# Kernel optimization log

Hardware: AMD Instinct MI355X
Metric: run time of the kernel (lower is better)

Reference implementation:

```python
import jax, jax.numpy as jnp
import numpy as np

ALPHA = -10.0  # softmax sharpness on |x - bin| distances
TAU = 0.0
TAU2 = 0.0
EPS = 1e-10

B, F, L, K = 32, 64, 1024, 32


def setup_inputs() -> dict:
    key = jax.random.key(0)
    k1, k2 = jax.random.split(key)
    x = jax.random.normal(k1, (B, F, L), dtype=jnp.float32)
    bins = jax.random.normal(k2, (K,), dtype=jnp.float32)
    return {"x": x, "bins": bins}


def reference(x, bins):
    # dist: [B, F, L, K] = |x[..., None] - bins|
    dist = jnp.abs(x[..., None] - bins)
    # soft assignment over the K bins (training path of the module)
    soft = jax.nn.softmax(ALPHA * dist, axis=-1)
    assignment = soft + EPS

    # weighted quantization loss: sum of per-bin mean of sqrt(assignment)
    quant = jnp.sum(jnp.mean(jnp.sqrt(assignment), axis=(0, 1, 2)))
    weighted_quant_loss = jnp.stack([quant, jnp.float32(TAU2)])[None, :]  # [1, 2]

    # code entropy of average assignment distribution
    p = jnp.mean(assignment, axis=(0, 1, 2))  # [K]
    code_entropy = -jnp.sum(p * jnp.log(p))
    weighted_code_entropy = jnp.stack([code_entropy, jnp.float32(TAU)])[None, :]  # [1, 2]

    # soft reconstruction against the bins: [B, F, L]
    bit_code = jnp.einsum('bflk,k->bfl', assignment, bins)
    return bit_code, weighted_code_entropy, weighted_quant_loss
```

## Files before the change

kernel.cpp:

```cpp
#include <hip/hip_runtime.h>

#define K      32
#define TPB    256
#define NB     2048
#define EPT    4
#define NTOT   (32 * 64 * 1024)
#define STRIDE (TPB * NB)

typedef float v2f __attribute__((ext_vector_type(2)));

__device__ __forceinline__ float wave_reduce_sum(float v) {
#pragma unroll
  for (int m = 1; m < 64; m <<= 1) v += __shfl_xor(v, m, 64);
  return v;
}

__device__ __forceinline__ float to_sgpr(float v) {
  return __int_as_float(__builtin_amdgcn_readfirstlane(__float_as_int(v)));
}

__global__ __launch_bounds__(TPB)
void ssq_main(const float* __restrict__ x, const float* __restrict__ bins,
              float* __restrict__ out, float* __restrict__ partials) {
  const int tid  = threadIdx.x;
  const int base = blockIdx.x * TPB + tid;

  float binv[K];
#pragma unroll
  for (int k = 0; k < K; ++k) binv[k] = to_sgpr(bins[k]);
  float binsum = 0.f;
#pragma unroll
  for (int k = 0; k < K; ++k) binsum += binv[k];
  const float epsb = 1e-10f * binsum;

  v2f binv2[K / 2];
#pragma unroll
  for (int i = 0; i < K / 2; ++i) binv2[i] = (v2f){binv[2 * i], binv[2 * i + 1]};

  float xs[EPT];
#pragma unroll
  for (int e = 0; e < EPT; ++e) xs[e] = x[base + e * STRIDE];

  v2f sAcc2[K / 2];
#pragma unroll
  for (int i = 0; i < K / 2; ++i) sAcc2[i] = (v2f){0.f, 0.f};
  float q = 0.f;

  const float Ch = -7.213475204444817f;
  const v2f Ch2 = {Ch, Ch};

#pragma unroll 1
  for (int e = 0; e < EPT; ++e) {
    const float xv = xs[e];
    const v2f xv2 = {xv, xv};
    v2f t2[K / 2];
    v2f s2a = {0.f, 0.f}, s2b = {0.f, 0.f};
    v2f h2a = {0.f, 0.f}, h2b = {0.f, 0.f};
    v2f b2a = {0.f, 0.f}, b2b = {0.f, 0.f};
#pragma unroll
    for (int i = 0; i < K / 2; i += 2) {
      v2f d0 = xv2 - binv2[i];
      v2f d1 = xv2 - binv2[i + 1];
      v2f p0 = d0 * Ch2;
      v2f p1 = d1 * Ch2;
      v2f m0 = __builtin_elementwise_min(p0, -p0);
      v2f m1 = __builtin_elementwise_min(p1, -p1);
      v2f h0 = {__builtin_amdgcn_exp2f(m0.x), __builtin_amdgcn_exp2f(m0.y)};
      v2f h1 = {__builtin_amdgcn_exp2f(m1.x), __builtin_amdgcn_exp2f(m1.y)};
      v2f t0 = h0 * h0;
      v2f t1 = h1 * h1;
      t2[i]     = t0;
      t2[i + 1] = t1;
      s2a += t0; s2b += t1;
      h2a += h0; h2b += h1;
      b2a += t0 * binv2[i];
      b2b += t1 * binv2[i + 1];
    }
    const v2f sv2 = (s2a + s2b);
    const v2f hv2 = (h2a + h2b);
    const v2f bv2 = (b2a + b2b);
    const float s    = sv2.x + sv2.y;
    const float hsum = hv2.x + hv2.y;
    const float bnum = bv2.x + bv2.y;
    const float inv  = __builtin_amdgcn_rcpf(s);
    q = fmaf(hsum, __builtin_amdgcn_rsqf(s), q);
    out[base + e * STRIDE] = fmaf(bnum, inv, epsb);
    const v2f inv2 = {inv, inv};
#pragma unroll
    for (int i = 0; i < K / 2; ++i) sAcc2[i] += t2[i] * inv2;
  }

  __shared__ float red[4][K + 1];
  const int lane = tid & 63, wv = tid >> 6;
#pragma unroll
  for (int k = 0; k < K; ++k) {
    float v = wave_reduce_sum(sAcc2[k >> 1][k & 1]);
    if (lane == 0) red[wv][k] = v;
  }
  {
    float v = wave_reduce_sum(q);
    if (lane == 0) red[wv][K] = v;
  }
  __syncthreads();
  if (tid < K + 1) {
    float v = red[0][tid] + red[1][tid] + red[2][tid] + red[3][tid];
    partials[tid * NB + blockIdx.x] = v;
  }
}

__global__ __launch_bounds__(TPB)
void ssq_reduce(const float* __restrict__ partials, float* __restrict__ sums) {
  const float* p = partials + blockIdx.x * NB;
  const int tid  = threadIdx.x;
  float s = 0.f;
#pragma unroll
  for (int j = 0; j < NB / TPB; ++j) s += p[tid + j * TPB];
  s = wave_reduce_sum(s);
  __shared__ float red[4];
  if ((tid & 63) == 0) red[tid >> 6] = s;
  __syncthreads();
  if (tid == 0) sums[blockIdx.x] = red[0] + red[1] + red[2] + red[3];
}

__global__ void ssq_final(const float* __restrict__ sums, float* __restrict__ out) {
  const int lane = threadIdx.x;
  float e = 0.f;
  if (lane < K) {
    float p = sums[lane] * (1.0f / (float)NTOT) + 1e-10f;
    e = -p * __logf(p);
  }
  e = wave_reduce_sum(e);
  if (lane == 0) {
    out[NTOT + 0] = e;
    out[NTOT + 1] = 0.f;
    out[NTOT + 2] = sums[K] * (1.0f / (float)NTOT);
    out[NTOT + 3] = 0.f;
  }
}

extern "C" void kernel_launch(void* const* d_in, const int* in_sizes, int n_in,
                              void* d_out, int out_size, void* d_ws, size_t ws_size,
                              hipStream_t stream) {
  const float* x    = (const float*)d_in[0];
  const float* bins = (const float*)d_in[1];
  float* out        = (float*)d_out;
  float* partials   = (float*)d_ws;
  float* sums       = partials + (K + 1) * NB;

  ssq_main  <<<NB,    TPB, 0, stream>>>(x, bins, out, partials);
  ssq_reduce<<<K + 1, TPB, 0, stream>>>(partials, sums);
  ssq_final <<<1,     64,  0, stream>>>(sums, out);
}
```

Baseline: 88.07 us.

## Fuse reduction kernels into main kernel via last-block atomic counter

Merges the three-kernel pipeline into a single kernel. Each block bumps an atomic counter after writing its partials, and the last block to finish reduces all partials and computes the entropy and quantization outputs. Halves the grid to 1024 blocks with 8 elements per thread so there are fewer partials, and unrolls the element loop by 2. This removes two kernel launches at the cost of a memset, a serial tail reduction run by one block, and higher register pressure from the unroll.

```diff
diff --git a/kernel.cpp b/kernel.cpp
--- a/kernel.cpp
+++ b/kernel.cpp
@@ -2,8 +2,8 @@
 
 #define K      32
 #define TPB    256
-#define NB     2048
-#define EPT    4
+#define NB     1024
+#define EPT    8
 #define NTOT   (32 * 64 * 1024)
 #define STRIDE (TPB * NB)
 
@@ -20,8 +20,9 @@
 }
 
 __global__ __launch_bounds__(TPB)
-void ssq_main(const float* __restrict__ x, const float* __restrict__ bins,
-              float* __restrict__ out, float* __restrict__ partials) {
+void ssq_fused(const float* __restrict__ x, const float* __restrict__ bins,
+               float* __restrict__ out, float* __restrict__ partials,
+               unsigned int* __restrict__ counter) {
   const int tid  = threadIdx.x;
   const int base = blockIdx.x * TPB + tid;
 
@@ -49,7 +50,7 @@
   const float Ch = -7.213475204444817f;
   const v2f Ch2 = {Ch, Ch};
 
-#pragma unroll 1
+#pragma unroll 2
   for (int e = 0; e < EPT; ++e) {
     const float xv = xs[e];
     const v2f xv2 = {xv, xv};
@@ -106,34 +107,36 @@
     float v = red[0][tid] + red[1][tid] + red[2][tid] + red[3][tid];
     partials[tid * NB + blockIdx.x] = v;
   }
-}
 
-__global__ __launch_bounds__(TPB)
-void ssq_reduce(const float* __restrict__ partials, float* __restrict__ sums) {
-  const float* p = partials + blockIdx.x * NB;
-  const int tid  = threadIdx.x;
-  float s = 0.f;
+  __shared__ unsigned int is_last;
+  __threadfence();
+  if (tid == 0) is_last = (atomicAdd(counter, 1u) == NB - 1u);
+  __syncthreads();
+  if (!is_last) return;
+  __threadfence();
+
+  __shared__ float sums[K + 1];
+  const int nrows = (wv == 3) ? 9 : 8;
+  for (int rr = 0; rr < nrows; ++rr) {
+    const int c = (rr < 8) ? (wv * 8 + rr) : K;
+    const float* p = partials + c * NB;
+    float sl = 0.f;
 #pragma unroll
-  for (int j = 0; j < NB / TPB; ++j) s += p[tid + j * TPB];
-  s = wave_reduce_sum(s);
-  __shared__ float red[4];
-  if ((tid & 63) == 0) red[tid >> 6] = s;
+    for (int j = 0; j < NB / 64; ++j) sl += p[lane + j * 64];
+    sl = wave_reduce_sum(sl);
+    if (lane == 0) sums[c] = sl;
+  }
   __syncthreads();
-  if (tid == 0) sums[blockIdx.x] = red[0] + red[1] + red[2] + red[3];
-}
-
-__global__ void ssq_final(const float* __restrict__ sums, float* __restrict__ out) {
-  const int lane = threadIdx.x;
-  float e = 0.f;
-  if (lane < K) {
-    float p = sums[lane] * (1.0f / (float)NTOT) + 1e-10f;
-    e = -p * __logf(p);
-  }
-  e = wave_reduce_sum(e);
-  if (lane == 0) {
-    out[NTOT + 0] = e;
+  if (tid == 0) {
+    const float invN = 1.0f / (float)NTOT;
+    float ent = 0.f;
+    for (int k = 0; k < K; ++k) {
+      float pk = sums[k] * invN + 1e-10f;
+      ent -= pk * __logf(pk);
+    }
+    out[NTOT + 0] = ent;
     out[NTOT + 1] = 0.f;
-    out[NTOT + 2] = sums[K] * (1.0f / (float)NTOT);
+    out[NTOT + 2] = sums[K] * invN;
     out[NTOT + 3] = 0.f;
   }
 }
@@ -145,9 +148,8 @@
   const float* bins = (const float*)d_in[1];
   float* out        = (float*)d_out;
   float* partials   = (float*)d_ws;
-  float* sums       = partials + (K + 1) * NB;
+  unsigned int* ctr = (unsigned int*)(partials + (K + 1) * NB);
 
-  ssq_main  <<<NB,    TPB, 0, stream>>>(x, bins, out, partials);
-  ssq_reduce<<<K + 1, TPB, 0, stream>>>(partials, sums);
-  ssq_final <<<1,     64,  0, stream>>>(sums, out);
+  hipMemsetAsync(ctr, 0, sizeof(unsigned int), stream);
+  ssq_fused<<<NB, TPB, 0, stream>>>(x, bins, out, partials, ctr);
 }
```

New measurement: 170.4 us. +93.5%, slower.
